# Performance work log

Hardware: AMD Instinct MI355X
Metric: run time of the kernel (lower is better)

## Reference

```python
import jax, jax.numpy as jnp
import numpy as np

EPS = 1e-12  # torch F.normalize eps


def _l2norm(x):
    n = jnp.linalg.norm(x, axis=-1, keepdims=True)
    return x / jnp.maximum(n, EPS)


def setup_inputs() -> dict:
    key = jax.random.key(0)
    k1, k2 = jax.random.split(key)
    B, Lq, Lk, D = 128, 32, 128, 128
    left_emb = jax.random.normal(k1, (B, Lq, D), dtype=jnp.float32)
    right_emb = jax.random.normal(k2, (B, Lk, D), dtype=jnp.float32)
    pos_idx = jnp.arange(B, dtype=jnp.int64)
    logit_scale = jnp.asarray(np.log(1.0 / 0.07), dtype=jnp.float32)  # scalar param
    return {"left_emb": left_emb, "right_emb": right_emb,
            "logit_scale": logit_scale, "pos_idx": pos_idx}


def reference(left_emb, right_emb, logit_scale, pos_idx):
    # maxsim_colbert: normalize token embeddings, cross-sim, max over doc
    # tokens, sum over query tokens -> [B, B] logits, then CE loss.
    l = _l2norm(left_emb)   # [B, Lq, D]
    r = _l2norm(right_emb)  # [B, Lk, D]
    sims = jnp.einsum('xik,yjk->xyij', l, r)        # [B, B, Lq, Lk]
    sim = sims.max(axis=-1).sum(axis=-1)            # [B, B]
    logits = jnp.exp(logit_scale) * sim
    logp = jax.nn.log_softmax(logits, axis=1)
    B = logits.shape[0]
    loss = -jnp.mean(logp[jnp.arange(B), pos_idx])
    return loss
```

## Files before the change

### kernel.cpp

```cpp
#include <hip/hip_runtime.h>
#include <hip/hip_bf16.h>

typedef short bf16x8 __attribute__((ext_vector_type(8)));
typedef float f32x16 __attribute__((ext_vector_type(16)));
typedef unsigned short u16;

#define B 128
#define LQ 32
#define LK 128
#define D 128
#define YPB 4
#define TILE_BYTES 32768


static __device__ inline u16 f2bf_rne(float f) {
  union { float f; unsigned u; } v; v.f = f;
  unsigned r = v.u + 0x7fffu + ((v.u >> 16) & 1u);
  return (u16)(r >> 16);
}

static __device__ inline unsigned swz(unsigned a) {
  return a ^ (((a >> 8) & 15u) << 4);
}

__global__ __launch_bounds__(256) void normalize_kernel(
    const float* __restrict__ left, const float* __restrict__ right,
    u16* __restrict__ l_out, u16* __restrict__ r_out) {
  int wave = (blockIdx.x * blockDim.x + threadIdx.x) >> 6;
  int lane = threadIdx.x & 63;
  const int n_l = B * LQ;
  const float* src; u16* dst; int row;
  if (wave < n_l) { src = left;  dst = l_out; row = wave; }
  else            { src = right; dst = r_out; row = wave - n_l; }
  float2 v = *reinterpret_cast<const float2*>(src + (size_t)row * D + lane * 2);
  float ss = v.x * v.x + v.y * v.y;
#pragma unroll
  for (int off = 1; off < 64; off <<= 1) ss += __shfl_xor(ss, off);
  float inv = 1.0f / fmaxf(sqrtf(ss), 1e-12f);
  unsigned packed = (unsigned)f2bf_rne(v.x * inv) |
                    ((unsigned)f2bf_rne(v.y * inv) << 16);
  *reinterpret_cast<unsigned*>(dst + (size_t)row * D + lane * 2) = packed;
}

__global__ __launch_bounds__(256, 2) void maxsim_kernel(
    const u16* __restrict__ lb, const u16* __restrict__ rb,
    float* __restrict__ sims) {
  __shared__ char smem[2 * TILE_BYTES];
  const int tid  = threadIdx.x;
  const int lane = tid & 63;
  const int wv   = tid >> 6;
  const int xg   = blockIdx.x >> 5;
  const int yg   = blockIdx.x & 31;
  const int x0   = xg * 8 + wv * 2;
  const unsigned rr = lane & 31;
  const unsigned hh = (unsigned)lane >> 5;

  {
    const char* ryb = (const char*)(rb + (size_t)(yg * YPB) * LK * D);
#pragma unroll
    for (int i = 0; i < 8; ++i) {
      unsigned Lrel = (unsigned)(i * 4096 + wv * 1024 + lane * 16);
      __builtin_amdgcn_global_load_lds(
          (const __attribute__((address_space(1))) void*)(ryb + swz(Lrel)),
          (__attribute__((address_space(3))) void*)(smem + i * 4096 + wv * 1024),
          16, 0, 0);
    }
  }

  unsigned kbase[8];
  const unsigned msk = rr & 15u;
#pragma unroll
  for (int ks = 0; ks < 8; ++ks)
    kbase[ks] = rr * 256u + (((((unsigned)ks << 1) | hh) ^ msk) << 4);

  bf16x8 bfr[2][8];
#pragma unroll
  for (int xi = 0; xi < 2; ++xi) {
    const u16* lx = lb + (size_t)(x0 + xi) * LQ * D + (size_t)rr * D;
#pragma unroll
    for (int ks = 0; ks < 8; ++ks)
      bfr[xi][ks] = *reinterpret_cast<const bf16x8*>(lx + ks * 16 + hh * 8);
  }

  f32x16 z;
#pragma unroll
  for (int t = 0; t < 16; ++t) z[t] = 0.f;

#pragma unroll
  for (int yy = 0; yy < YPB; ++yy) {
    if (yy + 1 < YPB) {
      const char* ryb = (const char*)(rb + (size_t)(yg * YPB + yy + 1) * LK * D);
      char* bufn = smem + ((yy + 1) & 1) * TILE_BYTES;
#pragma unroll
      for (int i = 0; i < 8; ++i) {
        unsigned Lrel = (unsigned)(i * 4096 + wv * 1024 + lane * 16);
        __builtin_amdgcn_global_load_lds(
            (const __attribute__((address_space(1))) void*)(ryb + swz(Lrel)),
            (__attribute__((address_space(3))) void*)(bufn + i * 4096 + wv * 1024),
            16, 0, 0);
      }
      asm volatile("s_waitcnt vmcnt(8)" ::: "memory");
    } else {
      asm volatile("s_waitcnt vmcnt(0)" ::: "memory");
    }
    asm volatile("s_barrier" ::: "memory");

    const char* buf = smem + (yy & 1) * TILE_BYTES;
    float cm0 = -3.0e38f, cm1 = -3.0e38f;

#pragma unroll
    for (int mj = 0; mj < 4; ++mj) {
      bf16x8 afr[8];
#pragma unroll
      for (int ks = 0; ks < 8; ++ks)
        afr[ks] = *reinterpret_cast<const bf16x8*>(buf + mj * 8192 + kbase[ks]);
      __builtin_amdgcn_s_setprio(1);
      f32x16 a0 = __builtin_amdgcn_mfma_f32_32x32x16_bf16(afr[0], bfr[0][0], z, 0, 0, 0);
      f32x16 a1 = __builtin_amdgcn_mfma_f32_32x32x16_bf16(afr[0], bfr[1][0], z, 0, 0, 0);
#pragma unroll
      for (int ks = 1; ks < 8; ++ks) {
        a0 = __builtin_amdgcn_mfma_f32_32x32x16_bf16(afr[ks], bfr[0][ks], a0, 0, 0, 0);
        a1 = __builtin_amdgcn_mfma_f32_32x32x16_bf16(afr[ks], bfr[1][ks], a1, 0, 0, 0);
      }
      __builtin_amdgcn_s_setprio(0);
      float t0, t1;
#pragma unroll
      for (int t = 0; t < 16; t += 4) {
        t0 = fmaxf(fmaxf(a0[t], a0[t + 1]), fmaxf(a0[t + 2], a0[t + 3]));
        t1 = fmaxf(fmaxf(a1[t], a1[t + 1]), fmaxf(a1[t + 2], a1[t + 3]));
        cm0 = fmaxf(cm0, t0);
        cm1 = fmaxf(cm1, t1);
      }
    }
    asm volatile("s_barrier" ::: "memory");

    const int y = yg * YPB + yy;
    cm0 = fmaxf(cm0, __shfl_xor(cm0, 32));
    cm1 = fmaxf(cm1, __shfl_xor(cm1, 32));
#pragma unroll
    for (int off = 1; off <= 16; off <<= 1) {
      cm0 += __shfl_xor(cm0, off);
      cm1 += __shfl_xor(cm1, off);
    }
    if (lane == 0) {
      sims[(x0 + 0) * B + y] = cm0;
      sims[(x0 + 1) * B + y] = cm1;
    }
  }
}

__global__ __launch_bounds__(1024) void loss_kernel(
    const float* __restrict__ sims, const float* __restrict__ logit_scale,
    const int* __restrict__ pos_idx, float* __restrict__ out) {
  __shared__ float red[16];
  const int lane = threadIdx.x & 63;
  const int wv   = threadIdx.x >> 6;
  const float scale = expf(logit_scale[0]);
  float local = 0.f;
#pragma unroll
  for (int rr = 0; rr < 8; ++rr) {
    const int x = wv * 8 + rr;
    const float* row = sims + x * B;
    float a = row[lane], b2 = row[64 + lane];
    float m = fmaxf(a, b2);
#pragma unroll
    for (int off = 1; off < 64; off <<= 1) m = fmaxf(m, __shfl_xor(m, off));
    float ml = scale * m;
    float e = expf(scale * a - ml) + expf(scale * b2 - ml);
#pragma unroll
    for (int off = 1; off < 64; off <<= 1) e += __shfl_xor(e, off);
    int pos = pos_idx[x];
    float pv = __shfl(pos < 64 ? a : b2, pos & 63);
    local += -(scale * pv - ml - logf(e));
  }
  if (lane == 0) red[wv] = local;
  __syncthreads();
  if (threadIdx.x == 0) {
    float t = 0.f;
#pragma unroll
    for (int i = 0; i < 16; ++i) t += red[i];
    out[0] = t / (float)B;
  }
}

extern "C" void kernel_launch(void* const* d_in, const int* in_sizes, int n_in,
                              void* d_out, int out_size, void* d_ws, size_t ws_size,
                              hipStream_t stream) {
  const float* left  = (const float*)d_in[0];
  const float* right = (const float*)d_in[1];
  const float* ls    = (const float*)d_in[2];
  const int*   pos   = (const int*)d_in[3];
  float* out = (float*)d_out;

  char* ws = (char*)d_ws;
  u16* lb   = (u16*)ws;
  u16* rbuf = (u16*)(ws + (size_t)B * LQ * D * 2);
  float* sims = (float*)(ws + (size_t)B * LQ * D * 2 + (size_t)B * LK * D * 2);

  int waves = B * LQ + B * LK;
  normalize_kernel<<<waves / 4, 256, 0, stream>>>(left, right, lb, rbuf);
  maxsim_kernel<<<512, 256, 0, stream>>>(lb, rbuf, sims);
  loss_kernel<<<1, 1024, 0, stream>>>(sims, ls, pos, out);
}
```

Measured before the change: 34.78 us.

## Pre-swizzle bf16 operands into MFMA fragment layout and drop LDS staging

The normalize kernel now writes the normalized bf16 embeddings directly in the per-lane MFMA fragment order, so each lane's 16-byte load is contiguous across the wave. The maxsim kernel drops the shared-memory double buffer, the global_load_lds copies and the barriers. It instead loads right-operand fragments straight from global memory into registers, with a two-slot register ping-pong that prefetches the next 32-row tile while MFMAs run. This removes LDS traffic and synchronisation, but each wave now re-reads the right tiles from global or L2 memory instead of sharing one LDS copy across the four waves.

Measured after the change: 35.78 us. 1.03x slower.

```diff
diff --git a/kernel.cpp b/kernel.cpp
--- a/kernel.cpp
+++ b/kernel.cpp
@@ -10,7 +10,6 @@
 #define LK 128
 #define D 128
 #define YPB 4
-#define TILE_BYTES 32768
 
 
 static __device__ inline u16 f2bf_rne(float f) {
@@ -19,122 +18,100 @@
   return (u16)(r >> 16);
 }
 
-static __device__ inline unsigned swz(unsigned a) {
-  return a ^ (((a >> 8) & 15u) << 4);
-}
-
 __global__ __launch_bounds__(256) void normalize_kernel(
     const float* __restrict__ left, const float* __restrict__ right,
-    u16* __restrict__ l_out, u16* __restrict__ r_out) {
+    char* __restrict__ lbf, char* __restrict__ rbf) {
   int wave = (blockIdx.x * blockDim.x + threadIdx.x) >> 6;
   int lane = threadIdx.x & 63;
   const int n_l = B * LQ;
-  const float* src; u16* dst; int row;
-  if (wave < n_l) { src = left;  dst = l_out; row = wave; }
-  else            { src = right; dst = r_out; row = wave - n_l; }
-  float2 v = *reinterpret_cast<const float2*>(src + (size_t)row * D + lane * 2);
+  const float* src; char* dst;
+  if (wave < n_l) {
+    int x = wave >> 5, i = wave & 31;
+    src = left + (size_t)wave * D;
+    dst = lbf + x * 8192 + i * 16;
+  } else {
+    int row = wave - n_l;
+    int y = row >> 7, j = row & 127;
+    src = right + (size_t)row * D;
+    dst = rbf + y * 32768 + (j >> 5) * 8192 + (j & 31) * 16;
+  }
+  float2 v = *reinterpret_cast<const float2*>(src + lane * 2);
   float ss = v.x * v.x + v.y * v.y;
 #pragma unroll
   for (int off = 1; off < 64; off <<= 1) ss += __shfl_xor(ss, off);
   float inv = 1.0f / fmaxf(sqrtf(ss), 1e-12f);
   unsigned packed = (unsigned)f2bf_rne(v.x * inv) |
                     ((unsigned)f2bf_rne(v.y * inv) << 16);
-  *reinterpret_cast<unsigned*>(dst + (size_t)row * D + lane * 2) = packed;
+  *reinterpret_cast<unsigned*>(
+      dst + (lane >> 3) * 1024 + ((lane >> 2) & 1) * 512 + (lane & 3) * 4) = packed;
 }
 
 __global__ __launch_bounds__(256, 2) void maxsim_kernel(
-    const u16* __restrict__ lb, const u16* __restrict__ rb,
+    const char* __restrict__ lbf, const char* __restrict__ rbf,
     float* __restrict__ sims) {
-  __shared__ char smem[2 * TILE_BYTES];
-  const int tid  = threadIdx.x;
-  const int lane = tid & 63;
-  const int wv   = tid >> 6;
+  const int lane = threadIdx.x & 63;
+  const int wv   = threadIdx.x >> 6;
   const int xg   = blockIdx.x >> 5;
   const int yg   = blockIdx.x & 31;
   const int x0   = xg * 8 + wv * 2;
-  const unsigned rr = lane & 31;
-  const unsigned hh = (unsigned)lane >> 5;
-
-  {
-    const char* ryb = (const char*)(rb + (size_t)(yg * YPB) * LK * D);
-#pragma unroll
-    for (int i = 0; i < 8; ++i) {
-      unsigned Lrel = (unsigned)(i * 4096 + wv * 1024 + lane * 16);
-      __builtin_amdgcn_global_load_lds(
-          (const __attribute__((address_space(1))) void*)(ryb + swz(Lrel)),
-          (__attribute__((address_space(3))) void*)(smem + i * 4096 + wv * 1024),
-          16, 0, 0);
-    }
-  }
-
-  unsigned kbase[8];
-  const unsigned msk = rr & 15u;
-#pragma unroll
-  for (int ks = 0; ks < 8; ++ks)
-    kbase[ks] = rr * 256u + (((((unsigned)ks << 1) | hh) ^ msk) << 4);
+  const int lane16 = lane * 16;
 
   bf16x8 bfr[2][8];
 #pragma unroll
-  for (int xi = 0; xi < 2; ++xi) {
-    const u16* lx = lb + (size_t)(x0 + xi) * LQ * D + (size_t)rr * D;
+  for (int xi = 0; xi < 2; ++xi)
 #pragma unroll
     for (int ks = 0; ks < 8; ++ks)
-      bfr[xi][ks] = *reinterpret_cast<const bf16x8*>(lx + ks * 16 + hh * 8);
-  }
+      bfr[xi][ks] = *reinterpret_cast<const bf16x8*>(
+          lbf + (x0 + xi) * 8192 + ks * 1024 + lane16);
 
   f32x16 z;
 #pragma unroll
   for (int t = 0; t < 16; ++t) z[t] = 0.f;
 
+  const char* rb0 = rbf + (size_t)(yg * YPB) * 32768;
+
+#define LOADA(dst, s_next)                                                   \
+  {                                                                          \
+    const char* nb = rb0 + ((s_next) >> 2) * 32768 + ((s_next) & 3) * 8192;  \
+    _Pragma("unroll")                                                        \
+    for (int ks = 0; ks < 8; ++ks)                                           \
+      dst[ks] = *reinterpret_cast<const bf16x8*>(nb + ks * 1024 + lane16);   \
+  }
+
+#define MFMAB(srcA)                                                          \
+  __builtin_amdgcn_s_setprio(1);                                             \
+  a0 = __builtin_amdgcn_mfma_f32_32x32x16_bf16(srcA[0], bfr[0][0], z, 0, 0, 0); \
+  a1 = __builtin_amdgcn_mfma_f32_32x32x16_bf16(srcA[0], bfr[1][0], z, 0, 0, 0); \
+  _Pragma("unroll")                                                          \
+  for (int ks = 1; ks < 8; ++ks) {                                           \
+    a0 = __builtin_amdgcn_mfma_f32_32x32x16_bf16(srcA[ks], bfr[0][ks], a0, 0, 0, 0); \
+    a1 = __builtin_amdgcn_mfma_f32_32x32x16_bf16(srcA[ks], bfr[1][ks], a1, 0, 0, 0); \
+  }                                                                          \
+  __builtin_amdgcn_s_setprio(0);
+
+  bf16x8 pA[8], pB[8];
+  LOADA(pA, 0);
+
 #pragma unroll
   for (int yy = 0; yy < YPB; ++yy) {
-    if (yy + 1 < YPB) {
-      const char* ryb = (const char*)(rb + (size_t)(yg * YPB + yy + 1) * LK * D);
-      char* bufn = smem + ((yy + 1) & 1) * TILE_BYTES;
-#pragma unroll
-      for (int i = 0; i < 8; ++i) {
-        unsigned Lrel = (unsigned)(i * 4096 + wv * 1024 + lane * 16);
-        __builtin_amdgcn_global_load_lds(
-            (const __attribute__((address_space(1))) void*)(ryb + swz(Lrel)),
-            (__attribute__((address_space(3))) void*)(bufn + i * 4096 + wv * 1024),
-            16, 0, 0);
-      }
-      asm volatile("s_waitcnt vmcnt(8)" ::: "memory");
-    } else {
-      asm volatile("s_waitcnt vmcnt(0)" ::: "memory");
-    }
-    asm volatile("s_barrier" ::: "memory");
-
-    const char* buf = smem + (yy & 1) * TILE_BYTES;
     float cm0 = -3.0e38f, cm1 = -3.0e38f;
-
 #pragma unroll
     for (int mj = 0; mj < 4; ++mj) {
-      bf16x8 afr[8];
-#pragma unroll
-      for (int ks = 0; ks < 8; ++ks)
-        afr[ks] = *reinterpret_cast<const bf16x8*>(buf + mj * 8192 + kbase[ks]);
-      __builtin_amdgcn_s_setprio(1);
-      f32x16 a0 = __builtin_amdgcn_mfma_f32_32x32x16_bf16(afr[0], bfr[0][0], z, 0, 0, 0);
-      f32x16 a1 = __builtin_amdgcn_mfma_f32_32x32x16_bf16(afr[0], bfr[1][0], z, 0, 0, 0);
-#pragma unroll
-      for (int ks = 1; ks < 8; ++ks) {
-        a0 = __builtin_amdgcn_mfma_f32_32x32x16_bf16(afr[ks], bfr[0][ks], a0, 0, 0, 0);
-        a1 = __builtin_amdgcn_mfma_f32_32x32x16_bf16(afr[ks], bfr[1][ks], a1, 0, 0, 0);
+      const int s = yy * 4 + mj;
+      f32x16 a0, a1;
+      if ((s & 1) == 0) {
+        if (s < 15) LOADA(pB, s + 1);
+        MFMAB(pA);
+      } else {
+        if (s < 15) LOADA(pA, s + 1);
+        MFMAB(pB);
       }
-      __builtin_amdgcn_s_setprio(0);
-      float t0, t1;
 #pragma unroll
       for (int t = 0; t < 16; t += 4) {
-        t0 = fmaxf(fmaxf(a0[t], a0[t + 1]), fmaxf(a0[t + 2], a0[t + 3]));
-        t1 = fmaxf(fmaxf(a1[t], a1[t + 1]), fmaxf(a1[t + 2], a1[t + 3]));
-        cm0 = fmaxf(cm0, t0);
-        cm1 = fmaxf(cm1, t1);
+        cm0 = fmaxf(cm0, fmaxf(fmaxf(a0[t], a0[t + 1]), fmaxf(a0[t + 2], a0[t + 3])));
+        cm1 = fmaxf(cm1, fmaxf(fmaxf(a1[t], a1[t + 1]), fmaxf(a1[t + 2], a1[t + 3])));
       }
     }
-    asm volatile("s_barrier" ::: "memory");
-
-    const int y = yg * YPB + yy;
     cm0 = fmaxf(cm0, __shfl_xor(cm0, 32));
     cm1 = fmaxf(cm1, __shfl_xor(cm1, 32));
 #pragma unroll
@@ -143,10 +120,13 @@
       cm1 += __shfl_xor(cm1, off);
     }
     if (lane == 0) {
+      const int y = yg * YPB + yy;
       sims[(x0 + 0) * B + y] = cm0;
       sims[(x0 + 1) * B + y] = cm1;
     }
   }
+#undef LOADA
+#undef MFMAB
 }
 
 __global__ __launch_bounds__(1024) void loss_kernel(
@@ -192,13 +172,13 @@
   const int*   pos   = (const int*)d_in[3];
   float* out = (float*)d_out;
 
-  char* ws = (char*)d_ws;
-  u16* lb   = (u16*)ws;
-  u16* rbuf = (u16*)(ws + (size_t)B * LQ * D * 2);
+  char* ws  = (char*)d_ws;
+  char* lbf = ws;
+  char* rbf = ws + (size_t)B * LQ * D * 2;
   float* sims = (float*)(ws + (size_t)B * LQ * D * 2 + (size_t)B * LK * D * 2);
 
   int waves = B * LQ + B * LK;
-  normalize_kernel<<<waves / 4, 256, 0, stream>>>(left, right, lb, rbuf);
-  maxsim_kernel<<<512, 256, 0, stream>>>(lb, rbuf, sims);
+  normalize_kernel<<<waves / 4, 256, 0, stream>>>(left, right, lbf, rbf);
+  maxsim_kernel<<<512, 256, 0, stream>>>(lbf, rbf, sims);
   loss_kernel<<<1, 1024, 0, stream>>>(sims, ls, pos, out);
 }
```
